# Performance work log

Hardware: AMD Instinct MI355X
Metric: run time of the kernel (lower is better)

## Reference

```python
import jax, jax.numpy as jnp
import numpy as np
from functools import partial

IN_DIM = 128
NUM_HEADS = 8
DOWN_DIM = IN_DIM // 2          # 64
HEAD_DIM = DOWN_DIM // NUM_HEADS  # 8
MID = max(1, DOWN_DIM // 16)    # 4 (gate_reduce=16)
DIL = 3
BN_EPS = 1e-5


def conv2d(x, w, padding=0, dilation=1):
    # x: [B,C,H,W], w: [O,I,kh,kw]
    return jax.lax.conv_general_dilated(
        x, w, window_strides=(1, 1),
        padding=[(padding, padding), (padding, padding)],
        rhs_dilation=(dilation, dilation),
        dimension_numbers=("NCHW", "OIHW", "NCHW"))


def batchnorm(x, gamma, beta, mean, var):
    # inference-mode BN over channel dim
    scale = (gamma / jnp.sqrt(var + BN_EPS))[None, :, None, None]
    shift = (beta - mean * gamma / jnp.sqrt(var + BN_EPS))[None, :, None, None]
    return x * scale + shift


def complex_l2_norm(z, eps=1e-6):
    denom = jnp.sqrt(jnp.sum(z.real ** 2 + z.imag ** 2, axis=-1, keepdims=True) + eps)
    return z / denom


def complex_softmax(z):
    return jax.lax.complex(jax.nn.softmax(z.real, axis=-1),
                           jax.nn.softmax(z.imag, axis=-1))


def setup_inputs() -> dict:
    key = jax.random.key(0)
    ks = jax.random.split(key, 6)
    B, H, W = 8, 128, 128
    inp = {}
    inp["x"] = jax.random.normal(ks[0], (B, IN_DIM, H, W), dtype=jnp.float32)
    inp["conv_w"] = jax.random.normal(ks[1], (DOWN_DIM, IN_DIM, 3, 3), dtype=jnp.float32) * 0.02
    inp["bn1_g"] = jnp.ones((DOWN_DIM,), jnp.float32)
    inp["bn1_b"] = jnp.zeros((DOWN_DIM,), jnp.float32)
    inp["bn1_m"] = jnp.zeros((DOWN_DIM,), jnp.float32)
    inp["bn1_v"] = jnp.ones((DOWN_DIM,), jnp.float32)
    inp["cg1_w"] = jax.random.normal(ks[2], (MID, DOWN_DIM, 1, 1), dtype=jnp.float32) * 0.1
    inp["cg1_b"] = jnp.zeros((MID,), jnp.float32)
    inp["cgbn_g"] = jnp.ones((MID,), jnp.float32)
    inp["cgbn_b"] = jnp.zeros((MID,), jnp.float32)
    inp["cgbn_m"] = jnp.zeros((MID,), jnp.float32)
    inp["cgbn_v"] = jnp.ones((MID,), jnp.float32)
    inp["cg2_w"] = jax.random.normal(ks[3], (DOWN_DIM, MID, 1, 1), dtype=jnp.float32) * 0.1
    inp["cg2_b"] = jnp.zeros((DOWN_DIM,), jnp.float32)
    inp["tau"] = jnp.ones((NUM_HEADS, 1, 1), jnp.float32) * (HEAD_DIM ** -0.5)
    return inp


def reference(x, conv_w, bn1_g, bn1_b, bn1_m, bn1_v,
              cg1_w, cg1_b, cgbn_g, cgbn_b, cgbn_m, cgbn_v,
              cg2_w, cg2_b, tau):
    B, C, H, W = x.shape
    # reduce branch: dilated 3x3 conv -> BN -> GELU (exact, matching torch nn.GELU)
    feat = conv2d(x, conv_w, padding=DIL, dilation=DIL)
    feat = batchnorm(feat, bn1_g, bn1_b, bn1_m, bn1_v)
    feat = jax.nn.gelu(feat, approximate=False)

    # q=k=v=g = fft2(feat) (torch computes four identical FFTs; same math)
    F2 = jnp.fft.fft2(feat.astype(jnp.float32), axes=(-2, -1))  # complex64 [B,64,H,W]
    N = H * W
    qkv = F2.reshape(B, NUM_HEADS, HEAD_DIM, N)  # b h d (H W)
    q = complex_l2_norm(qkv)
    k = complex_l2_norm(qkv)
    v = qkv
    # attn: [b,h,d,d] — tiny; contraction over N
    attn = jnp.einsum("bhdn,bhen->bhde", q, jnp.conj(k)) * tau
    attn = complex_softmax(attn)
    out_f = jnp.einsum("bhde,bhen->bhdn", attn, v)
    out_f = out_f.reshape(B, DOWN_DIM, H, W)
    out_f = jnp.abs(jnp.fft.ifft2(out_f, axes=(-2, -1)))

    # gated branch on g = F2
    gr = F2.real
    cg = conv2d(gr, cg1_w) + cg1_b[None, :, None, None]
    cg = batchnorm(cg, cgbn_g, cgbn_b, cgbn_m, cgbn_v)
    cg = jax.nn.gelu(cg, approximate=False)
    cg = conv2d(cg, cg2_w) + cg2_b[None, :, None, None]
    cg = jax.nn.sigmoid(cg)
    gate = cg * F2  # real gate times complex spectrum
    gate = jnp.abs(jnp.fft.ifft2(gate, axes=(-2, -1)))

    y = jnp.concatenate([out_f, gate], axis=1)
    return y + x
```

## Files before the change

### kernel.cpp

```cpp
#include <hip/hip_runtime.h>
#include <hip/hip_bf16.h>
#include <math.h>

#define NB 8
#define CIN 128
#define CDN 64
#define NPIX 16384
#define NHEADS 8
#define HDIM 8

typedef __attribute__((ext_vector_type(8))) short bf16x8;
typedef __attribute__((ext_vector_type(4))) float f32x4;
typedef __attribute__((ext_vector_type(8))) unsigned short u16x8;

struct alignas(8) c2 { float x, y; };

__device__ inline c2 cadd(c2 a, c2 b){ return {a.x+b.x, a.y+b.y}; }
__device__ inline c2 csub(c2 a, c2 b){ return {a.x-b.x, a.y-b.y}; }
__device__ inline c2 cmul(c2 a, c2 b){ return {a.x*b.x - a.y*b.y, a.x*b.y + a.y*b.x}; }
__device__ inline c2 shfl2(c2 v, int m){ return { __shfl_xor(v.x, m, 64), __shfl_xor(v.y, m, 64) }; }
__device__ inline float gelu_exact(float v){ return 0.5f*v*(1.f + erff(v*0.70710678118654752f)); }
__device__ inline unsigned short f2bf(float f){
  __hip_bfloat16 h = __float2bfloat16(f);
  return *reinterpret_cast<unsigned short*>(&h);
}

struct Tw { c2 t0; c2 t[6]; };
__device__ inline void tw_init(Tw& w, int t){
  float sn, cs;
  sincosf(-6.283185307179586f * (float)t * (1.f/128.f), &sn, &cs); w.t0 = {cs, sn};
  #pragma unroll
  for (int i = 0; i < 6; ++i) {
    int sp = 32 >> i;
    int j = t & (sp-1);
    sincosf(-3.141592653589793f * (float)j / (float)sp, &sn, &cs);
    w.t[i] = {cs, sn};
  }
}
__device__ inline void fft128_fwd(c2& a, c2& b, int t, const Tw& w){
  c2 s = cadd(a,b), d = csub(a,b);
  a = s; b = cmul(d, w.t0);
  #pragma unroll
  for (int i = 0; i < 6; ++i) {
    int sp = 32 >> i;
    c2 oa = shfl2(a, sp), ob = shfl2(b, sp);
    c2 tw = w.t[i];
    if (t & sp) { a = cmul(csub(oa,a), tw); b = cmul(csub(ob,b), tw); }
    else        { a = cadd(a,oa);           b = cadd(b,ob); }
  }
}
__device__ inline void fft128_inv(c2& a, c2& b, int t, const Tw& w){
  #pragma unroll
  for (int i = 5; i >= 0; --i) {
    int sp = 32 >> i;
    c2 tw = {w.t[i].x, -w.t[i].y};
    c2 oa = shfl2(a, sp), ob = shfl2(b, sp);
    if (t & sp) { a = csub(oa, cmul(a, tw)); b = csub(ob, cmul(b, tw)); }
    else        { a = cadd(a, cmul(oa, tw)); b = cadd(b, cmul(ob, tw)); }
  }
  c2 t0c = {w.t0.x, -w.t0.y};
  c2 wb = cmul(b, t0c);
  b = csub(a, wb);
  a = cadd(a, wb);
}

__device__ inline void gload_lds16(const void* g, void* l){
  __builtin_amdgcn_global_load_lds(
      (const __attribute__((address_space(1))) unsigned int*)g,
      (__attribute__((address_space(3))) unsigned int*)l, 16, 0, 0);
}

__device__ inline int colmap8(int wv, int i){
  if (wv == 0) return i;
  if (wv == 1) return 8 + i;
  if (wv == 2) return i < 4 ? 16 + i : 24 + i;
  if (wv == 3) return 20 + i;
  if (wv < 8) { int a = wv - 4; return i < 4 ? 32 + 4*a + i : 56 - 4*a + i; }
  int a = wv - 8; return i < 4 ? 64 + 4*a + i : 120 - 4*a + i;
}

__global__ __launch_bounds__(256) void k_wpack(const float* __restrict__ w, unsigned short* __restrict__ wP){
  int idx = blockIdx.x*256 + threadIdx.x;
  if (idx >= 4*9*64*32) return;
  int cc  = idx / 18432;
  int r   = idx - cc*18432;
  int tap = r / 2048;
  int r2  = r - tap*2048;
  int co  = r2 >> 5;
  int cil = r2 & 31;
  int ci  = cc*32 + cil;
  wP[idx] = f2bf(w[(co*CIN + ci)*9 + tap]);
}

__global__ __launch_bounds__(256) void k_xpose(const float* __restrict__ x, unsigned short* __restrict__ xT){
  int b = blockIdx.x >> 6;
  int px = (blockIdx.x & 63)*256 + threadIdx.x;
  const float* xb = x + (size_t)b*CIN*NPIX + px;
  #pragma unroll 2
  for (int ci0 = 0; ci0 < 128; ci0 += 8) {
    u16x8 v;
    #pragma unroll
    for (int j = 0; j < 8; ++j) v[j] = f2bf(xb[(size_t)(ci0+j)*NPIX]);
    int cc = ci0 >> 5;
    *(u16x8*)(xT + (((size_t)(b*4+cc)*NPIX + px)*32 + (ci0 & 31))) = v;
  }
}

__global__ __launch_bounds__(256) void k_conv(const unsigned short* __restrict__ xT,
    const unsigned short* __restrict__ wP,
    const float* __restrict__ bg, const float* __restrict__ bbeta,
    const float* __restrict__ bm, const float* __restrict__ bv,
    const float* __restrict__ w1,
    float* __restrict__ feat, float* __restrict__ u){
  __shared__ __align__(16) unsigned short sX[512*32];
  __shared__ float w1s[256];
  const int tid = threadIdx.x;
  const int bb   = blockIdx.z >> 1;
  const int half = blockIdx.z & 1;
  const int coBase = half*32;
  const int x0 = blockIdx.x * 16, y0 = blockIdx.y * 16;
  const int wv  = tid >> 6;
  const int l   = tid & 63;
  const int l15 = l & 15;
  const int g   = l >> 4;

  w1s[tid] = w1[tid];

  const bool interior = (x0 >= 16) && (x0 <= 96) && (y0 >= 16) && (y0 <= 96);

  f32x4 acc[2][4];
  #pragma unroll
  for (int m=0;m<2;++m)
    #pragma unroll
    for (int n=0;n<4;++n) acc[m][n] = {0.f,0.f,0.f,0.f};

  const int ko = g*8;

  for (int cc = 0; cc < 4; ++cc) {
    __syncthreads();
    const unsigned short* xcc = xT + ((size_t)(bb*4 + cc))*NPIX*32;
    if (interior) {
      #pragma unroll
      for (int k = 0; k < 8; ++k) {
        int blk = k*4 + wv;
        int idx = blk*64 + l;
        int p = idx >> 2, i = idx & 3;
        int pc = p < 484 ? p : 483;
        int py = pc / 22, px = pc - py*22;
        int gpix = (y0-3+py)*128 + (x0-3+px);
        int sg = i ^ ((p >> 1) & 3);
        const unsigned short* srcp = xcc + (size_t)gpix*32 + sg*8;
        gload_lds16(srcp, (char*)sX + blk*1024);
      }
    } else {
      #pragma unroll
      for (int k = 0; k < 8; ++k) {
        int idx = k*256 + tid;
        int p = idx >> 2, i = idx & 3;
        u16x8 v = {0,0,0,0,0,0,0,0};
        if (p < 484) {
          int py = p / 22, px = p - py*22;
          int gy = y0-3+py, gx = x0-3+px;
          if ((unsigned)gy < 128u && (unsigned)gx < 128u) {
            int sg = i ^ ((p >> 1) & 3);
            v = *(const u16x8*)(xcc + (size_t)(gy*128+gx)*32 + sg*8);
          }
        }
        *(u16x8*)((char*)sX + idx*16) = v;
      }
    }
    __syncthreads();

    const unsigned short* wcc = wP + cc*18432;
    for (int tap = 0; tap < 9; ++tap) {
      int dy = (tap/3)*3, dx = (tap - (tap/3)*3)*3;
      const unsigned short* wt = wcc + tap*2048;
      bf16x8 a[2], b[4];
      #pragma unroll
      for (int m = 0; m < 2; ++m)
        a[m] = *reinterpret_cast<const bf16x8*>(wt + (coBase + m*16 + l15)*32 + ko);
      #pragma unroll
      for (int n = 0; n < 4; ++n) {
        int p = (wv*4 + n + dy)*22 + l15 + dx;
        b[n] = *reinterpret_cast<const bf16x8*>(&sX[p*32 + ((g ^ ((p >> 1) & 3)) << 3)]);
      }
      #pragma unroll
      for (int m = 0; m < 2; ++m)
        #pragma unroll
        for (int n = 0; n < 4; ++n)
          acc[m][n] = __builtin_amdgcn_mfma_f32_16x16x32_bf16(a[m], b[n], acc[m][n], 0, 0, 0);
    }
  }

  float up[4][4];
  #pragma unroll
  for (int n=0;n<4;++n)
    #pragma unroll
    for (int m2=0;m2<4;++m2) up[n][m2] = 0.f;

  #pragma unroll
  for (int m = 0; m < 2; ++m) {
    #pragma unroll
    for (int r = 0; r < 4; ++r) {
      int co = coBase + m*16 + g*4 + r;
      float sc = bg[co] * rsqrtf(bv[co] + 1e-5f);
      float sh = bbeta[co] - bm[co]*sc;
      float wv4[4];
      #pragma unroll
      for (int m2 = 0; m2 < 4; ++m2) wv4[m2] = w1s[m2*64 + co];
      #pragma unroll
      for (int n = 0; n < 4; ++n) {
        int py = wv*4 + n;
        float v = gelu_exact(acc[m][n][r]*sc + sh);
        feat[((size_t)(bb*CDN + co)*128 + (y0+py))*128 + x0 + l15] = v;
        #pragma unroll
        for (int m2 = 0; m2 < 4; ++m2) up[n][m2] += wv4[m2]*v;
      }
    }
  }
  #pragma unroll
  for (int n=0;n<4;++n)
    #pragma unroll
    for (int m2=0;m2<4;++m2) {
      up[n][m2] += __shfl_xor(up[n][m2], 16, 64);
      up[n][m2] += __shfl_xor(up[n][m2], 32, 64);
    }
  if (g == 0) {
    #pragma unroll
    for (int n = 0; n < 4; ++n) {
      int py = y0 + wv*4 + n;
      #pragma unroll
      for (int m2 = 0; m2 < 4; ++m2)
        u[((size_t)((bb*2 + half)*4 + m2))*NPIX + py*128 + x0 + l15] = up[n][m2];
    }
  }
}

__global__ __launch_bounds__(256) void k_attn1(const float* __restrict__ feat, float* __restrict__ part){
  int bh = blockIdx.x, ck = blockIdx.y;
  int b = bh >> 3, h = bh & 7;
  const float* f = feat + (size_t)(b*CDN + h*HDIM)*NPIX;
  float acc[36];
  #pragma unroll
  for (int i=0;i<36;++i) acc[i]=0.f;
  for (int p = ck*2048 + threadIdx.x; p < (ck+1)*2048; p += 256) {
    float v[8];
    #pragma unroll
    for (int d=0; d<8; ++d) v[d] = f[d*NPIX + p];
    int i = 0;
    #pragma unroll
    for (int d=0; d<8; ++d)
      #pragma unroll
      for (int e=0; e<=d; ++e) acc[i++] += v[d]*v[e];
  }
  #pragma unroll
  for (int i=0;i<36;++i)
    #pragma unroll
    for (int off=32; off; off>>=1) acc[i] += __shfl_xor(acc[i], off, 64);
  __shared__ float red[4][36];
  int wave = threadIdx.x >> 6, lane = threadIdx.x & 63;
  if (lane == 0) {
    #pragma unroll
    for (int i=0;i<36;++i) red[wave][i] = acc[i];
  }
  __syncthreads();
  if (threadIdx.x < 36)
    part[(bh*8+ck)*36 + threadIdx.x] =
      red[0][threadIdx.x]+red[1][threadIdx.x]+red[2][threadIdx.x]+red[3][threadIdx.x];
}

__global__ __launch_bounds__(64) void k_attn2(const float* __restrict__ part, const float* __restrict__ tau,
                                              float* __restrict__ attn){
  int bh = blockIdx.x; int h = bh & 7;
  __shared__ float Gm[36];
  int i = threadIdx.x;
  if (i < 36) {
    float s = 0.f;
    #pragma unroll
    for (int k = 0; k < 8; ++k) s += part[(bh*8+k)*36 + i];
    Gm[i] = s;
  }
  __syncthreads();
  if (i == 0) {
    float G[8][8];
    int c=0;
    for (int d=0;d<8;++d) for(int e=0;e<=d;++e){
      float s = Gm[c]; G[d][e]=s; G[e][d]=s; ++c;
    }
    float nrm[8];
    for (int d=0;d<8;++d) nrm[d] = sqrtf(16384.f*G[d][d] + 1e-6f);
    float tv = tau[h];
    for (int d=0;d<8;++d) {
      float row[8]; float mx = -1e30f;
      for (int e=0;e<8;++e){ row[e] = tv*16384.f*G[d][e]/(nrm[d]*nrm[e]); mx = fmaxf(mx,row[e]); }
      float s=0.f;
      for (int e=0;e<8;++e){ row[e] = expf(row[e]-mx); s += row[e]; }
      for (int e=0;e<8;++e) attn[bh*64 + d*8 + e] = row[e]/s;
    }
  }
}

__global__ __launch_bounds__(256) void k_outf(const float* __restrict__ feat, const float* __restrict__ attn,
                                              const float* __restrict__ x, float* __restrict__ out){
  int bh = blockIdx.x; int b = bh >> 3, h = bh & 7;
  int p = blockIdx.y*256 + threadIdx.x;
  __shared__ float A[64];
  if (threadIdx.x < 64) A[threadIdx.x] = attn[bh*64 + threadIdx.x];
  __syncthreads();
  const float* f = feat + (size_t)(b*CDN + h*HDIM)*NPIX;
  float v[8];
  #pragma unroll
  for (int e=0;e<8;++e) v[e] = f[e*NPIX + p];
  float im = 0.f;
  #pragma unroll
  for (int e=0;e<8;++e) im += v[e];
  im *= 0.125f;
  #pragma unroll
  for (int d=0;d<8;++d){
    float re = 0.f;
    #pragma unroll
    for (int e=0;e<8;++e) re += A[d*8+e]*v[e];
    size_t o = ((size_t)(b*CIN + h*HDIM + d))*NPIX + p;
    out[o] = sqrtf(re*re + im*im) + x[o];
  }
}

__global__ __launch_bounds__(512) void k_ufft(const float* __restrict__ u,
    const float* __restrict__ b1,
    const float* __restrict__ gg, const float* __restrict__ gbeta,
    const float* __restrict__ gm, const float* __restrict__ gv,
    float* __restrict__ mid){
  __shared__ c2 T[64*129];
  int b = blockIdx.x >> 2, m = blockIdx.x & 3;
  int tid = threadIdx.x, wv = tid >> 6, t = tid & 63;
  Tw w; tw_init(w, t);
  const float* src0 = u + (size_t)((b*2+0)*4+m)*NPIX;
  const float* src1 = u + (size_t)((b*2+1)*4+m)*NPIX;
  c2 ra[16], rb[16];
  #pragma unroll
  for (int i = 0; i < 16; ++i) {
    int y = wv*16 + i;
    ra[i] = {src0[y*128 + t] + src1[y*128 + t], 0.f};
    rb[i] = {src0[y*128 + t + 64] + src1[y*128 + t + 64], 0.f};
  }
  #pragma unroll
  for (int i = 0; i < 16; ++i) fft128_fwd(ra[i], rb[i], t, w);
  c2 ca[16], cb[16];
  if (wv < 4) {
    #pragma unroll
    for (int i = 0; i < 16; ++i) {
      int y = wv*16 + i;
      T[y*129 + t] = ra[i]; T[y*129 + t + 64] = rb[i];
    }
  }
  __syncthreads();
  #pragma unroll
  for (int i = 0; i < 16; ++i) ca[i] = T[t*129 + wv*16 + i];
  __syncthreads();
  if (wv >= 4) {
    #pragma unroll
    for (int i = 0; i < 16; ++i) {
      int y = (wv-4)*16 + i;
      T[y*129 + t] = ra[i]; T[y*129 + t + 64] = rb[i];
    }
  }
  __syncthreads();
  #pragma unroll
  for (int i = 0; i < 16; ++i) cb[i] = T[t*129 + wv*16 + i];
  #pragma unroll
  for (int i = 0; i < 16; ++i) fft128_fwd(ca[i], cb[i], t, w);
  float sc = gg[m]*rsqrtf(gv[m]+1e-5f);
  float sh = gbeta[m] - gm[m]*sc;
  float bb1 = b1[m];
  float* md = mid + (size_t)(b*4+m)*NPIX;
  #pragma unroll
  for (int i = 0; i < 16; ++i) {
    int kx = wv*16 + i;
    md[kx*128 + t]      = gelu_exact((ca[i].x + bb1)*sc + sh);
    md[kx*128 + t + 64] = gelu_exact((cb[i].x + bb1)*sc + sh);
  }
}

__global__ __launch_bounds__(256) void k_gmap(const float* __restrict__ mid, const float* __restrict__ w2,
                                              const float* __restrict__ b2, unsigned* __restrict__ gPack){
  __shared__ float w2s[256], b2s[64];
  w2s[threadIdx.x] = w2[threadIdx.x];
  if (threadIdx.x < 64) b2s[threadIdx.x] = b2[threadIdx.x];
  __syncthreads();
  int b = blockIdx.x >> 6;
  int k = (blockIdx.x & 63)*256 + threadIdx.x;
  const float* md = mid + (size_t)b*4*NPIX + k;
  float m0 = md[0], m1 = md[NPIX], m2 = md[2*NPIX], m3 = md[3*NPIX];
  unsigned* gp = gPack + (size_t)b*32*NPIX + k;
  #pragma unroll 8
  for (int cp = 0; cp < 32; ++cp) {
    float slo = b2s[cp]    + w2s[cp*4]*m0    + w2s[cp*4+1]*m1    + w2s[cp*4+2]*m2    + w2s[cp*4+3]*m3;
    float shi = b2s[cp+32] + w2s[(cp+32)*4]*m0 + w2s[(cp+32)*4+1]*m1 + w2s[(cp+32)*4+2]*m2 + w2s[(cp+32)*4+3]*m3;
    slo = 1.f/(1.f+expf(-slo));
    shi = 1.f/(1.f+expf(-shi));
    gp[(size_t)cp*NPIX] = ((unsigned)f2bf(shi) << 16) | (unsigned)f2bf(slo);
  }
}

__global__ __launch_bounds__(1024)
void k_fused(const float* __restrict__ feat, const unsigned* __restrict__ gPack,
             const float* __restrict__ x, float* __restrict__ out){
  __shared__ c2 T[128*129];
  int ib = blockIdx.x;
  int b = ib >> 5, c = ib & 31;
  int tid = threadIdx.x, wv = tid >> 6, t = tid & 63;
  Tw w; tw_init(w, t);
  int ta = __brev((64 - (__brev(t) >> 26)) & 63) >> 26;
  const float* srcA = feat + (size_t)(b*CDN + c)*NPIX;
  const float* srcB = feat + (size_t)(b*CDN + c + 32)*NPIX;
  const unsigned* gp = gPack + (size_t)(b*32 + c)*NPIX;

  c2 ra[8], rb[8];
  #pragma unroll
  for (int i = 0; i < 8; ++i) {
    int y = wv*8 + i;
    ra[i] = {srcA[y*128 + t],      srcB[y*128 + t]};
    rb[i] = {srcA[y*128 + t + 64], srcB[y*128 + t + 64]};
  }
  #pragma unroll
  for (int i = 0; i < 8; ++i) fft128_fwd(ra[i], rb[i], t, w);
  #pragma unroll
  for (int i = 0; i < 8; ++i) {
    int y = wv*8 + i;
    T[y*129 + t] = ra[i]; T[y*129 + t + 64] = rb[i];
  }
  __syncthreads();
  c2 ca[8], cb[8];
  #pragma unroll
  for (int i = 0; i < 8; ++i) {
    int s = colmap8(wv, i);
    ca[i] = T[t*129 + s];
    cb[i] = T[(t+64)*129 + s];
  }
  unsigned gwa[8], gwb[8];
  #pragma unroll
  for (int i = 0; i < 8; ++i) {
    int s = colmap8(wv, i);
    gwa[i] = gp[s*128 + t];
    gwb[i] = gp[s*128 + 64 + t];
  }
  #pragma unroll
  for (int i = 0; i < 8; ++i) fft128_fwd(ca[i], cb[i], t, w);

  #define GUN(w_, lo_, hi_) float lo_ = __uint_as_float((w_) << 16); float hi_ = __uint_as_float((w_) & 0xffff0000u);
  #define CPAIR(I, J) { \
    GUN(gwa[I], g1aI, g2aI); GUN(gwb[I], g1bI, g2bI); \
    GUN(gwa[J], g1aJ, g2aJ); GUN(gwb[J], g1bJ, g2bJ); \
    c2 paI = { __shfl(ca[J].x, ta, 64), -__shfl(ca[J].y, ta, 64) }; \
    c2 paJ = { __shfl(ca[I].x, ta, 64), -__shfl(ca[I].y, ta, 64) }; \
    c2 pbI = { __shfl_xor(cb[J].x, 63, 64), -__shfl_xor(cb[J].y, 63, 64) }; \
    c2 pbJ = { __shfl_xor(cb[I].x, 63, 64), -__shfl_xor(cb[I].y, 63, 64) }; \
    float gsaI=0.5f*(g1aI+g2aI), gdaI=0.5f*(g1aI-g2aI); \
    float gsaJ=0.5f*(g1aJ+g2aJ), gdaJ=0.5f*(g1aJ-g2aJ); \
    float gsbI=0.5f*(g1bI+g2bI), gdbI=0.5f*(g1bI-g2bI); \
    float gsbJ=0.5f*(g1bJ+g2bJ), gdbJ=0.5f*(g1bJ-g2bJ); \
    ca[I] = { gsaI*ca[I].x + gdaI*paI.x, gsaI*ca[I].y + gdaI*paI.y }; \
    ca[J] = { gsaJ*ca[J].x + gdaJ*paJ.x, gsaJ*ca[J].y + gdaJ*paJ.y }; \
    cb[I] = { gsbI*cb[I].x + gdbI*pbI.x, gsbI*cb[I].y + gdbI*pbI.y }; \
    cb[J] = { gsbJ*cb[J].x + gdbJ*pbJ.x, gsbJ*cb[J].y + gdbJ*pbJ.y }; \
  }
  #define CSELF(I) { \
    GUN(gwa[I], g1aI, g2aI); GUN(gwb[I], g1bI, g2bI); \
    c2 paI = { __shfl(ca[I].x, ta, 64), -__shfl(ca[I].y, ta, 64) }; \
    c2 pbI = { __shfl_xor(cb[I].x, 63, 64), -__shfl_xor(cb[I].y, 63, 64) }; \
    float gsaI=0.5f*(g1aI+g2aI), gdaI=0.5f*(g1aI-g2aI); \
    float gsbI=0.5f*(g1bI+g2bI), gdbI=0.5f*(g1bI-g2bI); \
    ca[I] = { gsaI*ca[I].x + gdaI*paI.x, gsaI*ca[I].y + gdaI*paI.y }; \
    cb[I] = { gsbI*cb[I].x + gdbI*pbI.x, gsbI*cb[I].y + gdbI*pbI.y }; \
  }
  if (wv == 0) {
    CSELF(0); CSELF(1);
    CPAIR(2,3); CPAIR(4,7); CPAIR(5,6);
  } else {
    CPAIR(0,7); CPAIR(1,6); CPAIR(2,5); CPAIR(3,4);
  }
  #undef CPAIR
  #undef CSELF
  #undef GUN

  #pragma unroll
  for (int i = 0; i < 8; ++i) fft128_inv(ca[i], cb[i], t, w);
  __syncthreads();
  #pragma unroll
  for (int i = 0; i < 8; ++i) {
    int s = colmap8(wv, i);
    T[t*129 + s] = ca[i];
    T[(t+64)*129 + s] = cb[i];
  }
  __syncthreads();
  #pragma unroll
  for (int i = 0; i < 8; ++i) {
    int y = wv*8 + i;
    ra[i] = T[y*129 + t];
    rb[i] = T[y*129 + t + 64];
  }
  #pragma unroll
  for (int i = 0; i < 8; ++i) fft128_inv(ra[i], rb[i], t, w);
  const float* xr1 = x + ((size_t)(b*CIN + 64 + c))*NPIX;
  const float* xr2 = x + ((size_t)(b*CIN + 96 + c))*NPIX;
  float* o1 = out + ((size_t)(b*CIN + 64 + c))*NPIX;
  float* o2 = out + ((size_t)(b*CIN + 96 + c))*NPIX;
  const float s = 1.f/16384.f;
  #pragma unroll
  for (int i = 0; i < 8; ++i) {
    int y = wv*8 + i;
    o1[y*128 + t]      = fabsf(ra[i].x)*s + xr1[y*128 + t];
    o1[y*128 + t + 64] = fabsf(rb[i].x)*s + xr1[y*128 + t + 64];
    o2[y*128 + t]      = fabsf(ra[i].y)*s + xr2[y*128 + t];
    o2[y*128 + t + 64] = fabsf(rb[i].y)*s + xr2[y*128 + t + 64];
  }
}

extern "C" void kernel_launch(void* const* d_in, const int* in_sizes, int n_in,
                              void* d_out, int out_size, void* d_ws, size_t ws_size,
                              hipStream_t stream){
  const float* x      = (const float*)d_in[0];
  const float* conv_w = (const float*)d_in[1];
  const float* bn1_g  = (const float*)d_in[2];
  const float* bn1_b  = (const float*)d_in[3];
  const float* bn1_m  = (const float*)d_in[4];
  const float* bn1_v  = (const float*)d_in[5];
  const float* cg1_w  = (const float*)d_in[6];
  const float* cg1_b  = (const float*)d_in[7];
  const float* cgbn_g = (const float*)d_in[8];
  const float* cgbn_b = (const float*)d_in[9];
  const float* cgbn_m = (const float*)d_in[10];
  const float* cgbn_v = (const float*)d_in[11];
  const float* cg2_w  = (const float*)d_in[12];
  const float* cg2_b  = (const float*)d_in[13];
  const float* tau    = (const float*)d_in[14];
  float* out = (float*)d_out;

  char* ws = (char*)d_ws;
  float*          feat  = (float*)ws;
  unsigned short* xT    = (unsigned short*)(ws + 33554432);
  unsigned*       gPack = (unsigned*)(ws + 33554432);
  float*          u     = (float*)(ws + 67108864);
  float*          mid   = (float*)(ws + 71303168);
  unsigned short* wPack = (unsigned short*)(ws + 73400320);
  float*          attn  = (float*)(ws + 73547776);
  float*          part  = (float*)(ws + 73564160);

  k_wpack<<<288, 256, 0, stream>>>(conv_w, wPack);
  k_xpose<<<512, 256, 0, stream>>>(x, xT);
  k_conv<<<dim3(8,8,NB*2), 256, 0, stream>>>(xT, wPack, bn1_g, bn1_b, bn1_m, bn1_v, cg1_w, feat, u);
  k_ufft<<<NB*4, 512, 0, stream>>>(u, cg1_b, cgbn_g, cgbn_b, cgbn_m, cgbn_v, mid);
  k_gmap<<<NB*64, 256, 0, stream>>>(mid, cg2_w, cg2_b, gPack);
  k_attn1<<<dim3(NB*NHEADS, 8), 256, 0, stream>>>(feat, part);
  k_attn2<<<NB*NHEADS, 64, 0, stream>>>(part, tau, attn);
  k_outf<<<dim3(NB*NHEADS, 64), 256, 0, stream>>>(feat, attn, x, out);
  k_fused<<<NB*32, 1024, 0, stream>>>(feat, gPack, x, out);
}
```

Measured before the change: 208.6 us.

## Store conv feature map in bf16 and remap conv grid for adjacent channel halves

The post-conv GELU feature map is written as bf16 instead of fp32 and widened back to float on load in the attention, output and fused FFT kernels. This halves the feature-map bytes written once and read three times. The conv launch grid is also reordered so both channel halves of a tile come from neighbouring blocks, which should help L2 reuse of the shared input tile. The cost is reduced precision of the intermediate feeding the FFTs and the Gram matrix. The 16-bit loads are also narrower per lane and may coalesce less efficiently.

```diff
diff --git a/kernel.cpp b/kernel.cpp
--- a/kernel.cpp
+++ b/kernel.cpp
@@ -24,6 +24,7 @@
   __hip_bfloat16 h = __float2bfloat16(f);
   return *reinterpret_cast<unsigned short*>(&h);
 }
+__device__ inline float bf2f(unsigned short u){ return __uint_as_float((unsigned)u << 16); }
 
 struct Tw { c2 t0; c2 t[6]; };
 __device__ inline void tw_init(Tw& w, int t){
@@ -111,14 +112,14 @@
     const float* __restrict__ bg, const float* __restrict__ bbeta,
     const float* __restrict__ bm, const float* __restrict__ bv,
     const float* __restrict__ w1,
-    float* __restrict__ feat, float* __restrict__ u){
+    unsigned short* __restrict__ feat, float* __restrict__ u){
   __shared__ __align__(16) unsigned short sX[512*32];
   __shared__ float w1s[256];
   const int tid = threadIdx.x;
-  const int bb   = blockIdx.z >> 1;
-  const int half = blockIdx.z & 1;
+  const int bb   = blockIdx.z;
+  const int half = blockIdx.x & 1;
   const int coBase = half*32;
-  const int x0 = blockIdx.x * 16, y0 = blockIdx.y * 16;
+  const int x0 = (blockIdx.x >> 1) * 16, y0 = blockIdx.y * 16;
   const int wv  = tid >> 6;
   const int l   = tid & 63;
   const int l15 = l & 15;
@@ -212,7 +213,7 @@
       for (int n = 0; n < 4; ++n) {
         int py = wv*4 + n;
         float v = gelu_exact(acc[m][n][r]*sc + sh);
-        feat[((size_t)(bb*CDN + co)*128 + (y0+py))*128 + x0 + l15] = v;
+        feat[((size_t)(bb*CDN + co)*128 + (y0+py))*128 + x0 + l15] = f2bf(v);
         #pragma unroll
         for (int m2 = 0; m2 < 4; ++m2) up[n][m2] += wv4[m2]*v;
       }
@@ -236,17 +237,17 @@
   }
 }
 
-__global__ __launch_bounds__(256) void k_attn1(const float* __restrict__ feat, float* __restrict__ part){
+__global__ __launch_bounds__(256) void k_attn1(const unsigned short* __restrict__ feat, float* __restrict__ part){
   int bh = blockIdx.x, ck = blockIdx.y;
   int b = bh >> 3, h = bh & 7;
-  const float* f = feat + (size_t)(b*CDN + h*HDIM)*NPIX;
+  const unsigned short* f = feat + (size_t)(b*CDN + h*HDIM)*NPIX;
   float acc[36];
   #pragma unroll
   for (int i=0;i<36;++i) acc[i]=0.f;
   for (int p = ck*2048 + threadIdx.x; p < (ck+1)*2048; p += 256) {
     float v[8];
     #pragma unroll
-    for (int d=0; d<8; ++d) v[d] = f[d*NPIX + p];
+    for (int d=0; d<8; ++d) v[d] = bf2f(f[d*NPIX + p]);
     int i = 0;
     #pragma unroll
     for (int d=0; d<8; ++d)
@@ -300,17 +301,17 @@
   }
 }
 
-__global__ __launch_bounds__(256) void k_outf(const float* __restrict__ feat, const float* __restrict__ attn,
+__global__ __launch_bounds__(256) void k_outf(const unsigned short* __restrict__ feat, const float* __restrict__ attn,
                                               const float* __restrict__ x, float* __restrict__ out){
   int bh = blockIdx.x; int b = bh >> 3, h = bh & 7;
   int p = blockIdx.y*256 + threadIdx.x;
   __shared__ float A[64];
   if (threadIdx.x < 64) A[threadIdx.x] = attn[bh*64 + threadIdx.x];
   __syncthreads();
-  const float* f = feat + (size_t)(b*CDN + h*HDIM)*NPIX;
+  const unsigned short* f = feat + (size_t)(b*CDN + h*HDIM)*NPIX;
   float v[8];
   #pragma unroll
-  for (int e=0;e<8;++e) v[e] = f[e*NPIX + p];
+  for (int e=0;e<8;++e) v[e] = bf2f(f[e*NPIX + p]);
   float im = 0.f;
   #pragma unroll
   for (int e=0;e<8;++e) im += v[e];
@@ -403,7 +404,7 @@
 }
 
 __global__ __launch_bounds__(1024)
-void k_fused(const float* __restrict__ feat, const unsigned* __restrict__ gPack,
+void k_fused(const unsigned short* __restrict__ feat, const unsigned* __restrict__ gPack,
              const float* __restrict__ x, float* __restrict__ out){
   __shared__ c2 T[128*129];
   int ib = blockIdx.x;
@@ -411,16 +412,16 @@
   int tid = threadIdx.x, wv = tid >> 6, t = tid & 63;
   Tw w; tw_init(w, t);
   int ta = __brev((64 - (__brev(t) >> 26)) & 63) >> 26;
-  const float* srcA = feat + (size_t)(b*CDN + c)*NPIX;
-  const float* srcB = feat + (size_t)(b*CDN + c + 32)*NPIX;
+  const unsigned short* srcA = feat + (size_t)(b*CDN + c)*NPIX;
+  const unsigned short* srcB = feat + (size_t)(b*CDN + c + 32)*NPIX;
   const unsigned* gp = gPack + (size_t)(b*32 + c)*NPIX;
 
   c2 ra[8], rb[8];
   #pragma unroll
   for (int i = 0; i < 8; ++i) {
     int y = wv*8 + i;
-    ra[i] = {srcA[y*128 + t],      srcB[y*128 + t]};
-    rb[i] = {srcA[y*128 + t + 64], srcB[y*128 + t + 64]};
+    ra[i] = {bf2f(srcA[y*128 + t]),      bf2f(srcB[y*128 + t])};
+    rb[i] = {bf2f(srcA[y*128 + t + 64]), bf2f(srcB[y*128 + t + 64])};
   }
   #pragma unroll
   for (int i = 0; i < 8; ++i) fft128_fwd(ra[i], rb[i], t, w);
@@ -537,7 +538,7 @@
   float* out = (float*)d_out;
 
   char* ws = (char*)d_ws;
-  float*          feat  = (float*)ws;
+  unsigned short* feat  = (unsigned short*)ws;
   unsigned short* xT    = (unsigned short*)(ws + 33554432);
   unsigned*       gPack = (unsigned*)(ws + 33554432);
   float*          u     = (float*)(ws + 67108864);
@@ -548,7 +549,7 @@
 
   k_wpack<<<288, 256, 0, stream>>>(conv_w, wPack);
   k_xpose<<<512, 256, 0, stream>>>(x, xT);
-  k_conv<<<dim3(8,8,NB*2), 256, 0, stream>>>(xT, wPack, bn1_g, bn1_b, bn1_m, bn1_v, cg1_w, feat, u);
+  k_conv<<<dim3(16,8,NB), 256, 0, stream>>>(xT, wPack, bn1_g, bn1_b, bn1_m, bn1_v, cg1_w, feat, u);
   k_ufft<<<NB*4, 512, 0, stream>>>(u, cg1_b, cgbn_g, cgbn_b, cgbn_m, cgbn_v, mid);
   k_gmap<<<NB*64, 256, 0, stream>>>(mid, cg2_w, cg2_b, gPack);
   k_attn1<<<dim3(NB*NHEADS, 8), 256, 0, stream>>>(feat, part);
```

Result: no change. 206.1 us (-1.2%).
